# Kernel optimization log

Measured on AMD Instinct MI355X. Metric: run time of the kernel, lower is better.

Reference implementation:

```python
import jax, jax.numpy as jnp
import numpy as np

NUM_HEADS = 16
NUM_HIDDENS = 1024
D_K = NUM_HIDDENS // NUM_HEADS
NEG_INF = -1.0e9


def setup_inputs() -> dict:
    key = jax.random.key(0)
    kx, kq, kk, kv, ko, kl = jax.random.split(key, 6)
    B, S, D = 2, 2048, NUM_HIDDENS
    scale = 1.0 / np.sqrt(D)
    return {
        "X": jax.random.normal(kx, (B, S, D), dtype=jnp.float32),
        "valid_lens": jax.random.randint(kl, (B,), 0, S, dtype=jnp.int64),
        "W_q": jax.random.normal(kq, (D, D), dtype=jnp.float32) * scale,
        "W_k": jax.random.normal(kk, (D, D), dtype=jnp.float32) * scale,
        "W_v": jax.random.normal(kv, (D, D), dtype=jnp.float32) * scale,
        "W_o": jax.random.normal(ko, (D, D), dtype=jnp.float32) * scale,
    }


def _split_heads(x):
    # [B, S, D] -> [B, H, S, d_k]
    B, S, _ = x.shape
    return x.reshape(B, S, NUM_HEADS, D_K).transpose(0, 2, 1, 3)


def reference(X, valid_lens, W_q, W_k, W_v, W_o):
    B, S, D = X.shape
    # nn.Linear(bias=False): y = x @ W.T  (W is [out, in])
    Q = _split_heads(jnp.einsum("bsd,ed->bse", X, W_q))  # [B,H,S,dk]
    K = _split_heads(jnp.einsum("bsd,ed->bse", X, W_k))
    V = _split_heads(jnp.einsum("bsd,ed->bse", X, W_v))

    scores = jnp.einsum("bhqd,bhkd->bhqk", Q, K) / jnp.sqrt(
        jnp.asarray(D_K, dtype=X.dtype)
    )  # [B,H,S,S]

    # key-position mask per batch: positions >= valid_len get -1e9
    mask = jnp.arange(S)[None, :] >= valid_lens[:, None]  # [B,S]
    scores = jnp.where(mask[:, None, None, :], jnp.asarray(NEG_INF, X.dtype), scores)

    attn = jax.nn.softmax(scores, axis=-1)  # dropout p=0 -> identity
    out = jnp.einsum("bhqk,bhkd->bhqd", attn, V)  # [B,H,S,dk]
    out = out.transpose(0, 2, 1, 3).reshape(B, S, D)
    return jnp.einsum("bsd,ed->bse", out, W_o)
```

## Files before the change

### kernel.cpp

```cpp
#include <hip/hip_runtime.h>
#include <stdint.h>

#define S_LEN 2048
#define BATCH 2
#define DMODEL 1024
#define NHEAD 16
#define DK 64
#define MROWS (BATCH * S_LEN)

typedef __attribute__((ext_vector_type(8))) short bf16x8;
typedef __attribute__((ext_vector_type(4))) float f32x4;
typedef __attribute__((ext_vector_type(4))) short short4v;
typedef __attribute__((ext_vector_type(2))) uint32_t u32x2;

__device__ __forceinline__ short f2b(float f) {
    union { float f; uint32_t u; } c; c.f = f;
    uint32_t u = c.u;
    return (short)((u + 0x7fffu + ((u >> 16) & 1u)) >> 16);
}

__device__ __forceinline__ void gload16(const void* g, void* l) {
    __builtin_amdgcn_global_load_lds(
        (const __attribute__((address_space(1))) void*)g,
        (__attribute__((address_space(3))) void*)l, 16, 0, 0);
}

__global__ void cvt_kernel(const float* __restrict__ X, const float* __restrict__ Wq,
                           const float* __restrict__ Wk, const float* __restrict__ Wv,
                           const float* __restrict__ Wo,
                           short* __restrict__ Xb, short* __restrict__ Wqb,
                           short* __restrict__ Wkb, short* __restrict__ Wvb,
                           short* __restrict__ Wob) {
    const float* src; short* dst; int n4;
    switch (blockIdx.y) {
        case 0:  src = X;  dst = Xb;  n4 = MROWS * DMODEL / 4;  break;
        case 1:  src = Wq; dst = Wqb; n4 = DMODEL * DMODEL / 4; break;
        case 2:  src = Wk; dst = Wkb; n4 = DMODEL * DMODEL / 4; break;
        case 3:  src = Wv; dst = Wvb; n4 = DMODEL * DMODEL / 4; break;
        default: src = Wo; dst = Wob; n4 = DMODEL * DMODEL / 4; break;
    }
    for (int i = blockIdx.x * blockDim.x + threadIdx.x; i < n4;
         i += gridDim.x * blockDim.x) {
        float4 v = ((const float4*)src)[i];
        short4v o;
        o[0] = f2b(v.x); o[1] = f2b(v.y); o[2] = f2b(v.z); o[3] = f2b(v.w);
        ((short4v*)dst)[i] = o;
    }
}

template <int OUT_F32>
__global__ __launch_bounds__(256) void gemm_bt(
    const short* __restrict__ A,
    const short* __restrict__ Bt0, const short* __restrict__ Bt1,
    const short* __restrict__ Bt2,
    short* __restrict__ Cb0, short* __restrict__ Cb1, short* __restrict__ Cb2,
    float* __restrict__ Cf, int M, int N, int K) {
    __shared__ short sA[2][128 * 32];
    __shared__ short sB[2][128 * 32];

    const short* Bt = Bt0;
    short* Cb = Cb0;
    if (blockIdx.z == 1) { Bt = Bt1; Cb = Cb1; }
    else if (blockIdx.z == 2) { Bt = Bt2; Cb = Cb2; }

    const int tid = threadIdx.x;
    const int lane = tid & 63;
    const int wid = tid >> 6;
    const int wr = wid >> 1, wc = wid & 1;
    const int brow = blockIdx.y * 128;
    const int bcol = blockIdx.x * 128;
    const int lr = lane & 15;
    const int kh = (lane >> 4) << 3;
    const int swg = ((lr >> 1) & 3) << 3;
    const int khs = kh ^ swg;

    f32x4 acc[4][4] = {};

    const int idx0 = tid, idx1 = tid + 256;
    const int ar0 = idx0 >> 2, ak0 = ((idx0 & 3) << 3) ^ (((ar0 >> 1) & 3) << 3);
    const int ar1 = idx1 >> 2, ak1 = ((idx1 & 3) << 3) ^ (((ar1 >> 1) & 3) << 3);

    const short* gA0 = A + (size_t)(brow + ar0) * K + ak0;
    const short* gA1 = A + (size_t)(brow + ar1) * K + ak1;
    const short* gB0 = Bt + (size_t)(bcol + ar0) * K + ak0;
    const short* gB1 = Bt + (size_t)(bcol + ar1) * K + ak1;

    const int nk = K >> 5;
    gload16(gA0, &sA[0][idx0 * 8]);
    gload16(gA1, &sA[0][idx1 * 8]);
    gload16(gB0, &sB[0][idx0 * 8]);
    gload16(gB1, &sB[0][idx1 * 8]);
    __syncthreads();

    int cur = 0;
    for (int kt = 0; kt < nk; ++kt) {
        if (kt + 1 < nk) {
            const int k0 = (kt + 1) << 5;
            gload16(gA0 + k0, &sA[cur ^ 1][idx0 * 8]);
            gload16(gA1 + k0, &sA[cur ^ 1][idx1 * 8]);
            gload16(gB0 + k0, &sB[cur ^ 1][idx0 * 8]);
            gload16(gB1 + k0, &sB[cur ^ 1][idx1 * 8]);
        }

        bf16x8 a[4], b[4];
#pragma unroll
        for (int mt = 0; mt < 4; ++mt)
            a[mt] = *(const bf16x8*)&sA[cur][(wr * 64 + mt * 16 + lr) * 32 + khs];
#pragma unroll
        for (int nt = 0; nt < 4; ++nt)
            b[nt] = *(const bf16x8*)&sB[cur][(wc * 64 + nt * 16 + lr) * 32 + khs];
        __builtin_amdgcn_s_setprio(1);
#pragma unroll
        for (int mt = 0; mt < 4; ++mt)
#pragma unroll
            for (int nt = 0; nt < 4; ++nt)
                acc[mt][nt] = __builtin_amdgcn_mfma_f32_16x16x32_bf16(
                    a[mt], b[nt], acc[mt][nt], 0, 0, 0);
        __builtin_amdgcn_s_setprio(0);

        __syncthreads();
        cur ^= 1;
    }

    const int rbase = (lane >> 4) << 2;
    const bool vtrans = (!OUT_F32) && (blockIdx.z == 2);
#pragma unroll
    for (int mt = 0; mt < 4; ++mt) {
#pragma unroll
        for (int nt = 0; nt < 4; ++nt) {
            if (vtrans) {
                int row0 = brow + wr * 64 + mt * 16 + rbase;
                int col = bcol + wc * 64 + nt * 16 + lr;
                int bb = row0 >> 11, key = row0 & 2047;
                int hh = col >> 6, d = col & 63;
                short4v pk;
#pragma unroll
                for (int j = 0; j < 4; ++j) pk[j] = f2b(acc[mt][nt][j]);
                *(short4v*)&Cb[((size_t)((bb * 16 + hh) * 64 + d)) * S_LEN + key] = pk;
            } else {
#pragma unroll
                for (int j = 0; j < 4; ++j) {
                    int row = brow + wr * 64 + mt * 16 + rbase + j;
                    int col = bcol + wc * 64 + nt * 16 + lr;
                    if (OUT_F32)
                        Cf[(size_t)row * N + col] = acc[mt][nt][j];
                    else
                        Cb[(size_t)row * N + col] = f2b(acc[mt][nt][j]);
                }
            }
        }
    }
}

__global__ __launch_bounds__(128, 4) void attn_kernel(
    const short* __restrict__ Q, const short* __restrict__ K,
    const short* __restrict__ Vt, short* __restrict__ O,
    const int* __restrict__ vlens) {
    __shared__ short sK[2][64 * 64];
    __shared__ short sV[2][64 * 64];
    __shared__ short sP[2][2][16 * 64];

    const int tid = threadIdx.x;
    const int lane = tid & 63;
    const int w = tid >> 6;
    const int id = blockIdx.x;
    const int id2 = ((id & 7) << 7) | (id >> 3);
    const int qb = id2 & 31;
    const int bhx = id2 >> 5;
    const int b = bhx & 1, h = bhx >> 1;
    const int lr = lane & 15;
    const int kh = (lane >> 4) << 3;
    const int rbase = (lane >> 4) << 2;
    const int swq = (lr & 7) << 3;

    int vl = vlens[b];
    if (vl < 0) vl = 0;
    if (vl > S_LEN) vl = S_LEN;
    const bool allm = (vl == 0);
    if (allm) vl = S_LEN;
    const int nT = (vl + 63) >> 6;
    const int nFull = ((vl & 63) == 0) ? nT : nT - 1;

    const size_t rowbase = (size_t)(b * S_LEN) * DMODEL + h * DK;
    const short* vt = Vt + ((size_t)((b * 16 + h) * 64)) * S_LEN;

    const short* qrowA = Q + rowbase + (size_t)(qb * 64 + w * 32 + lr) * DMODEL;
    const short* qrowB = qrowA + 16 * DMODEL;
    bf16x8 qf0a = *(const bf16x8*)(qrowA + kh);
    bf16x8 qf1a = *(const bf16x8*)(qrowA + 32 + kh);
    bf16x8 qf0b = *(const bf16x8*)(qrowB + kh);
    bf16x8 qf1b = *(const bf16x8*)(qrowB + 32 + kh);
    if (allm) {
#pragma unroll
        for (int i = 0; i < 8; ++i) { qf0a[i] = 0; qf1a[i] = 0; qf0b[i] = 0; qf1b[i] = 0; }
    }

    f32x4 oacA[4] = {}, oacB[4] = {};
    float mA = -1e30f, mcA = -1e30f, lA = 0.f;
    float mB = -1e30f, mcB = -1e30f, lB = 0.f;
    const float CEXP = 0.18033688011112042f;
    const float THRADD = 44.361419556f;

    const int lofs0 = lr * 64 + (kh ^ swq);
    const int lofs1 = lr * 64 + ((32 + kh) ^ swq);

    const int r0 = tid >> 3;
    const int kc = (((tid & 7) ^ (r0 & 7)) << 3);
    const short* kP = K + rowbase + (size_t)r0 * DMODEL + kc;
    const short* vP = vt + (size_t)r0 * S_LEN + kc;

#pragma unroll
    for (int i = 0; i < 4; ++i) {
        gload16(kP + (size_t)(i * 16) * DMODEL, &sK[0][(tid + i * 128) * 8]);
        gload16(vP + (size_t)(i * 16) * S_LEN, &sV[0][(tid + i * 128) * 8]);
    }
    __syncthreads();

#define SOFTMAX_FRAG(SACC, MRUN, MC, LRUN, OAC, SPW)                            \
    do {                                                                        \
        float t0 = fmaxf(fmaxf(SACC[0][0], SACC[0][1]), SACC[0][2]);            \
        float t1 = fmaxf(fmaxf(SACC[0][3], SACC[1][0]), SACC[1][1]);            \
        float t2 = fmaxf(fmaxf(SACC[1][2], SACC[1][3]), SACC[2][0]);            \
        float t3 = fmaxf(fmaxf(SACC[2][1], SACC[2][2]), SACC[2][3]);            \
        float t4 = fmaxf(fmaxf(SACC[3][0], SACC[3][1]), SACC[3][2]);            \
        float pmax = fmaxf(fmaxf(fmaxf(t0, t1), t2),                            \
                           fmaxf(fmaxf(t3, t4), SACC[3][3]));                   \
        if (__any(pmax > MRUN + THRADD)) {                                      \
            float mx = pmax;                                                    \
            mx = fmaxf(mx, __shfl_xor(mx, 16));                                 \
            mx = fmaxf(mx, __shfl_xor(mx, 32));                                 \
            float scl = __builtin_exp2f((MRUN - mx) * CEXP);                    \
            MRUN = mx;                                                          \
            MC = mx * CEXP;                                                     \
            LRUN *= scl;                                                        \
            _Pragma("unroll")                                                   \
            for (int dt = 0; dt < 4; ++dt)                                      \
                _Pragma("unroll")                                               \
                for (int j = 0; j < 4; ++j) OAC[dt][j] *= scl;                  \
        }                                                                       \
        float p[16];                                                            \
        _Pragma("unroll")                                                       \
        for (int nt = 0; nt < 4; ++nt)                                          \
            _Pragma("unroll")                                                   \
            for (int j = 0; j < 4; ++j)                                         \
                p[nt * 4 + j] = __builtin_exp2f(                                \
                    __builtin_fmaf(SACC[nt][j], CEXP, -MC));                    \
        float ls = ((p[0] + p[1]) + (p[2] + p[3])) +                            \
                   ((p[4] + p[5]) + (p[6] + p[7]));                             \
        ls += ((p[8] + p[9]) + (p[10] + p[11])) +                               \
              ((p[12] + p[13]) + (p[14] + p[15]));                              \
        LRUN += ls;                                                             \
        _Pragma("unroll")                                                       \
        for (int nt = 0; nt < 4; ++nt) {                                        \
            u32x2 r;                                                            \
            asm("v_cvt_pk_bf16_f32 %0, %1, %2"                                  \
                : "=v"(r[0]) : "v"(p[nt * 4 + 0]), "v"(p[nt * 4 + 1]));         \
            asm("v_cvt_pk_bf16_f32 %0, %1, %2"                                  \
                : "=v"(r[1]) : "v"(p[nt * 4 + 2]), "v"(p[nt * 4 + 3]));         \
            *(u32x2*)&SPW[lr * 64 + ((nt * 16 + rbase) ^ swq)] = r;             \
        }                                                                       \
    } while (0)

#define TILE_BODY(MASKED_C)                                                     \
    do {                                                                        \
        constexpr bool MASKED = MASKED_C;                                       \
        const short* sKc = sK[cur];                                             \
        const short* sVc = sV[cur];                                             \
        const short* kL0 = sKc + lofs0;                                         \
        const short* kL1 = sKc + lofs1;                                         \
        f32x4 saccA[4] = {}, saccB[4] = {};                                     \
        __builtin_amdgcn_s_setprio(1);                                          \
        _Pragma("unroll")                                                       \
        for (int nt = 0; nt < 4; ++nt) {                                        \
            bf16x8 kb0 = *(const bf16x8*)&kL0[nt * 1024];                       \
            bf16x8 kb1 = *(const bf16x8*)&kL1[nt * 1024];                       \
            saccA[nt] = __builtin_amdgcn_mfma_f32_16x16x32_bf16(                \
                kb0, qf0a, saccA[nt], 0, 0, 0);                                 \
            saccB[nt] = __builtin_amdgcn_mfma_f32_16x16x32_bf16(                \
                kb0, qf0b, saccB[nt], 0, 0, 0);                                 \
            saccA[nt] = __builtin_amdgcn_mfma_f32_16x16x32_bf16(                \
                kb1, qf1a, saccA[nt], 0, 0, 0);                                 \
            saccB[nt] = __builtin_amdgcn_mfma_f32_16x16x32_bf16(                \
                kb1, qf1b, saccB[nt], 0, 0, 0);                                 \
        }                                                                       \
        __builtin_amdgcn_s_setprio(0);                                          \
        if (MASKED) {                                                           \
            _Pragma("unroll")                                                   \
            for (int nt = 0; nt < 4; ++nt)                                      \
                _Pragma("unroll")                                               \
                for (int j = 0; j < 4; ++j) {                                   \
                    int keyi = t * 64 + nt * 16 + rbase + j;                    \
                    if (keyi >= vl) { saccA[nt][j] = -3.0e38f;                  \
                                      saccB[nt][j] = -3.0e38f; }                \
                }                                                               \
        }                                                                       \
        SOFTMAX_FRAG(saccA, mA, mcA, lA, oacA, (&sP[w][0][0]));                 \
        SOFTMAX_FRAG(saccB, mB, mcB, lB, oacB, (&sP[w][1][0]));                 \
        const short* vL0 = sVc + lofs0;                                         \
        const short* vL1 = sVc + lofs1;                                         \
        __builtin_amdgcn_s_setprio(1);                                          \
        {                                                                       \
            bf16x8 pfA = *(const bf16x8*)&sP[w][0][lofs0];                      \
            bf16x8 pfB = *(const bf16x8*)&sP[w][1][lofs0];                      \
            _Pragma("unroll")                                                   \
            for (int dt = 0; dt < 4; ++dt) {                                    \
                bf16x8 vf = *(const bf16x8*)&vL0[dt * 1024];                    \
                oacA[dt] = __builtin_amdgcn_mfma_f32_16x16x32_bf16(             \
                    vf, pfA, oacA[dt], 0, 0, 0);                                \
                oacB[dt] = __builtin_amdgcn_mfma_f32_16x16x32_bf16(             \
                    vf, pfB, oacB[dt], 0, 0, 0);                                \
            }                                                                   \
            pfA = *(const bf16x8*)&sP[w][0][lofs1];                             \
            pfB = *(const bf16x8*)&sP[w][1][lofs1];                             \
            _Pragma("unroll")                                                   \
            for (int dt = 0; dt < 4; ++dt) {                                    \
                bf16x8 vf = *(const bf16x8*)&vL1[dt * 1024];                    \
                oacA[dt] = __builtin_amdgcn_mfma_f32_16x16x32_bf16(             \
                    vf, pfA, oacA[dt], 0, 0, 0);                                \
                oacB[dt] = __builtin_amdgcn_mfma_f32_16x16x32_bf16(             \
                    vf, pfB, oacB[dt], 0, 0, 0);                                \
            }                                                                   \
        }                                                                       \
        __builtin_amdgcn_s_setprio(0);                                          \
    } while (0)

    int cur = 0;
    for (int t = 0; t < nT; ++t) {
        const bool hn = (t + 1 < nT);
        if (hn) {
            short* sKn = sK[cur ^ 1];
            short* sVn = sV[cur ^ 1];
            kP += 64 * DMODEL;
            vP += 64;
#pragma unroll
            for (int i = 0; i < 4; ++i) {
                gload16(kP + (size_t)(i * 16) * DMODEL, &sKn[(tid + i * 128) * 8]);
                gload16(vP + (size_t)(i * 16) * S_LEN, &sVn[(tid + i * 128) * 8]);
            }
        }

        if (t < nFull) TILE_BODY(false);
        else TILE_BODY(true);

        __syncthreads();
        cur ^= 1;
    }
#undef TILE_BODY
#undef SOFTMAX_FRAG

    float ltA = lA + __shfl_xor(lA, 16);
    ltA += __shfl_xor(ltA, 32);
    float rlA = 1.f / ltA;
    float ltB = lB + __shfl_xor(lB, 16);
    ltB += __shfl_xor(ltB, 32);
    float rlB = 1.f / ltB;

    short* orowA = O + rowbase + (size_t)(qb * 64 + w * 32 + lr) * DMODEL;
    short* orowB = orowA + 16 * DMODEL;
#pragma unroll
    for (int dt = 0; dt < 4; ++dt) {
        short4v pkA, pkB;
#pragma unroll
        for (int j = 0; j < 4; ++j) {
            pkA[j] = f2b(oacA[dt][j] * rlA);
            pkB[j] = f2b(oacB[dt][j] * rlB);
        }
        *(short4v*)&orowA[dt * 16 + rbase] = pkA;
        *(short4v*)&orowB[dt * 16 + rbase] = pkB;
    }
}

extern "C" void kernel_launch(void* const* d_in, const int* in_sizes, int n_in,
                              void* d_out, int out_size, void* d_ws, size_t ws_size,
                              hipStream_t stream) {
    const float* X = (const float*)d_in[0];
    const int* vlens = (const int*)d_in[1];
    const float* Wq = (const float*)d_in[2];
    const float* Wk = (const float*)d_in[3];
    const float* Wv = (const float*)d_in[4];
    const float* Wo = (const float*)d_in[5];
    float* out = (float*)d_out;

    short* Xb = (short*)d_ws;
    short* Wqb = Xb + (size_t)MROWS * DMODEL;
    short* Wkb = Wqb + (size_t)DMODEL * DMODEL;
    short* Wvb = Wkb + (size_t)DMODEL * DMODEL;
    short* Wob = Wvb + (size_t)DMODEL * DMODEL;
    short* Qb = Wob + (size_t)DMODEL * DMODEL;
    short* Kb = Qb + (size_t)MROWS * DMODEL;
    short* Vtb = Kb + (size_t)MROWS * DMODEL;
    short* Ob = Vtb + (size_t)MROWS * DMODEL;

    cvt_kernel<<<dim3(512, 5), 256, 0, stream>>>(X, Wq, Wk, Wv, Wo, Xb, Wqb, Wkb,
                                                 Wvb, Wob);
    gemm_bt<0><<<dim3(8, 32, 3), 256, 0, stream>>>(Xb, Wqb, Wkb, Wvb, Qb, Kb, Vtb,
                                                   nullptr, MROWS, DMODEL, DMODEL);
    attn_kernel<<<dim3(1024), 128, 0, stream>>>(Qb, Kb, Vtb, Ob, vlens);
    gemm_bt<1><<<dim3(8, 32, 1), 256, 0, stream>>>(Ob, Wob, Wob, Wob, nullptr,
                                                   nullptr, nullptr, out, MROWS,
                                                   DMODEL, DMODEL);
}
```

Measured before the change: 107.4 us.

## Load K/V fragments directly from global memory in single-wave attention blocks

The attention kernel switches from 2-wave blocks that stage K and V tiles in double-buffered LDS via async global-to-LDS loads to single-wave blocks that read K and V MFMA fragments straight from global memory. This removes LDS staging and the per-tile __syncthreads, and doubles the grid with a new XCD-aware block mapping so each XCD handles whole (batch, head) pairs. In exchange, K/V reuse across waves now depends on L2/L1 caches, the loads are strided row reads with no software prefetch, and global load latency sits directly in front of the MFMAs.

Result: slower. 166.0 us (+54.6%).

```diff
diff --git a/kernel.cpp b/kernel.cpp
--- a/kernel.cpp
+++ b/kernel.cpp
@@ -152,21 +152,19 @@
     }
 }
 
-__global__ __launch_bounds__(128, 4) void attn_kernel(
+__global__ __launch_bounds__(64, 4) void attn_kernel(
     const short* __restrict__ Q, const short* __restrict__ K,
     const short* __restrict__ Vt, short* __restrict__ O,
     const int* __restrict__ vlens) {
-    __shared__ short sK[2][64 * 64];
-    __shared__ short sV[2][64 * 64];
-    __shared__ short sP[2][2][16 * 64];
-
-    const int tid = threadIdx.x;
-    const int lane = tid & 63;
-    const int w = tid >> 6;
+    __shared__ short sP[2][16 * 64];
+
+    const int lane = threadIdx.x;
     const int id = blockIdx.x;
-    const int id2 = ((id & 7) << 7) | (id >> 3);
-    const int qb = id2 & 31;
-    const int bhx = id2 >> 5;
+    const int xcd = id & 7;
+    const int k_ = id >> 3;
+    const int qb = k_ & 63;
+    const int g = k_ >> 6;
+    const int bhx = xcd + 8 * g;
     const int b = bhx & 1, h = bhx >> 1;
     const int lr = lane & 15;
     const int kh = (lane >> 4) << 3;
@@ -184,7 +182,7 @@
     const size_t rowbase = (size_t)(b * S_LEN) * DMODEL + h * DK;
     const short* vt = Vt + ((size_t)((b * 16 + h) * 64)) * S_LEN;
 
-    const short* qrowA = Q + rowbase + (size_t)(qb * 64 + w * 32 + lr) * DMODEL;
+    const short* qrowA = Q + rowbase + (size_t)(qb * 32 + lr) * DMODEL;
     const short* qrowB = qrowA + 16 * DMODEL;
     bf16x8 qf0a = *(const bf16x8*)(qrowA + kh);
     bf16x8 qf1a = *(const bf16x8*)(qrowA + 32 + kh);
@@ -201,20 +199,11 @@
     const float CEXP = 0.18033688011112042f;
     const float THRADD = 44.361419556f;
 
+    const short* kRun = K + rowbase + (size_t)lr * DMODEL + kh;
+    const short* vRun = vt + (size_t)lr * S_LEN + kh;
+
     const int lofs0 = lr * 64 + (kh ^ swq);
     const int lofs1 = lr * 64 + ((32 + kh) ^ swq);
-
-    const int r0 = tid >> 3;
-    const int kc = (((tid & 7) ^ (r0 & 7)) << 3);
-    const short* kP = K + rowbase + (size_t)r0 * DMODEL + kc;
-    const short* vP = vt + (size_t)r0 * S_LEN + kc;
-
-#pragma unroll
-    for (int i = 0; i < 4; ++i) {
-        gload16(kP + (size_t)(i * 16) * DMODEL, &sK[0][(tid + i * 128) * 8]);
-        gload16(vP + (size_t)(i * 16) * S_LEN, &sV[0][(tid + i * 128) * 8]);
-    }
-    __syncthreads();
 
 #define SOFTMAX_FRAG(SACC, MRUN, MC, LRUN, OAC, SPW)                            \
     do {                                                                        \
@@ -264,16 +253,12 @@
 #define TILE_BODY(MASKED_C)                                                     \
     do {                                                                        \
         constexpr bool MASKED = MASKED_C;                                       \
-        const short* sKc = sK[cur];                                             \
-        const short* sVc = sV[cur];                                             \
-        const short* kL0 = sKc + lofs0;                                         \
-        const short* kL1 = sKc + lofs1;                                         \
         f32x4 saccA[4] = {}, saccB[4] = {};                                     \
         __builtin_amdgcn_s_setprio(1);                                          \
         _Pragma("unroll")                                                       \
         for (int nt = 0; nt < 4; ++nt) {                                        \
-            bf16x8 kb0 = *(const bf16x8*)&kL0[nt * 1024];                       \
-            bf16x8 kb1 = *(const bf16x8*)&kL1[nt * 1024];                       \
+            bf16x8 kb0 = *(const bf16x8*)(kRun + (size_t)(nt * 16) * DMODEL);   \
+            bf16x8 kb1 = *(const bf16x8*)(kRun + (size_t)(nt * 16) * DMODEL + 32); \
             saccA[nt] = __builtin_amdgcn_mfma_f32_16x16x32_bf16(                \
                 kb0, qf0a, saccA[nt], 0, 0, 0);                                 \
             saccB[nt] = __builtin_amdgcn_mfma_f32_16x16x32_bf16(                \
@@ -294,27 +279,25 @@
                                       saccB[nt][j] = -3.0e38f; }                \
                 }                                                               \
         }                                                                       \
-        SOFTMAX_FRAG(saccA, mA, mcA, lA, oacA, (&sP[w][0][0]));                 \
-        SOFTMAX_FRAG(saccB, mB, mcB, lB, oacB, (&sP[w][1][0]));                 \
-        const short* vL0 = sVc + lofs0;                                         \
-        const short* vL1 = sVc + lofs1;                                         \
+        SOFTMAX_FRAG(saccA, mA, mcA, lA, oacA, (&sP[0][0]));                    \
+        SOFTMAX_FRAG(saccB, mB, mcB, lB, oacB, (&sP[1][0]));                    \
         __builtin_amdgcn_s_setprio(1);                                          \
         {                                                                       \
-            bf16x8 pfA = *(const bf16x8*)&sP[w][0][lofs0];                      \
-            bf16x8 pfB = *(const bf16x8*)&sP[w][1][lofs0];                      \
+            bf16x8 pfA = *(const bf16x8*)&sP[0][lofs0];                         \
+            bf16x8 pfB = *(const bf16x8*)&sP[1][lofs0];                         \
             _Pragma("unroll")                                                   \
             for (int dt = 0; dt < 4; ++dt) {                                    \
-                bf16x8 vf = *(const bf16x8*)&vL0[dt * 1024];                    \
+                bf16x8 vf = *(const bf16x8*)(vRun + (size_t)(dt * 16) * S_LEN); \
                 oacA[dt] = __builtin_amdgcn_mfma_f32_16x16x32_bf16(             \
                     vf, pfA, oacA[dt], 0, 0, 0);                                \
                 oacB[dt] = __builtin_amdgcn_mfma_f32_16x16x32_bf16(             \
                     vf, pfB, oacB[dt], 0, 0, 0);                                \
             }                                                                   \
-            pfA = *(const bf16x8*)&sP[w][0][lofs1];                             \
-            pfB = *(const bf16x8*)&sP[w][1][lofs1];                             \
+            pfA = *(const bf16x8*)&sP[0][lofs1];                                \
+            pfB = *(const bf16x8*)&sP[1][lofs1];                                \
             _Pragma("unroll")                                                   \
             for (int dt = 0; dt < 4; ++dt) {                                    \
-                bf16x8 vf = *(const bf16x8*)&vL1[dt * 1024];                    \
+                bf16x8 vf = *(const bf16x8*)(vRun + (size_t)(dt * 16) * S_LEN + 32); \
                 oacA[dt] = __builtin_amdgcn_mfma_f32_16x16x32_bf16(             \
                     vf, pfA, oacA[dt], 0, 0, 0);                                \
                 oacB[dt] = __builtin_amdgcn_mfma_f32_16x16x32_bf16(             \
@@ -324,26 +307,11 @@
         __builtin_amdgcn_s_setprio(0);                                          \
     } while (0)
 
-    int cur = 0;
     for (int t = 0; t < nT; ++t) {
-        const bool hn = (t + 1 < nT);
-        if (hn) {
-            short* sKn = sK[cur ^ 1];
-            short* sVn = sV[cur ^ 1];
-            kP += 64 * DMODEL;
-            vP += 64;
-#pragma unroll
-            for (int i = 0; i < 4; ++i) {
-                gload16(kP + (size_t)(i * 16) * DMODEL, &sKn[(tid + i * 128) * 8]);
-                gload16(vP + (size_t)(i * 16) * S_LEN, &sVn[(tid + i * 128) * 8]);
-            }
-        }
-
         if (t < nFull) TILE_BODY(false);
         else TILE_BODY(true);
-
-        __syncthreads();
-        cur ^= 1;
+        kRun += 64 * DMODEL;
+        vRun += 64;
     }
 #undef TILE_BODY
 #undef SOFTMAX_FRAG
@@ -355,7 +323,7 @@
     ltB += __shfl_xor(ltB, 32);
     float rlB = 1.f / ltB;
 
-    short* orowA = O + rowbase + (size_t)(qb * 64 + w * 32 + lr) * DMODEL;
+    short* orowA = O + rowbase + (size_t)(qb * 32 + lr) * DMODEL;
     short* orowB = orowA + 16 * DMODEL;
 #pragma unroll
     for (int dt = 0; dt < 4; ++dt) {
@@ -395,7 +363,7 @@
                                                  Wvb, Wob);
     gemm_bt<0><<<dim3(8, 32, 3), 256, 0, stream>>>(Xb, Wqb, Wkb, Wvb, Qb, Kb, Vtb,
                                                    nullptr, MROWS, DMODEL, DMODEL);
-    attn_kernel<<<dim3(1024), 128, 0, stream>>>(Qb, Kb, Vtb, Ob, vlens);
+    attn_kernel<<<dim3(2048), 64, 0, stream>>>(Qb, Kb, Vtb, Ob, vlens);
     gemm_bt<1><<<dim3(8, 32, 1), 256, 0, stream>>>(Ob, Wob, Wob, Wob, nullptr,
                                                    nullptr, nullptr, out, MROWS,
                                                    DMODEL, DMODEL);
```
